# Kernel optimization log

Measured on AMD Instinct MI355X. Metric: run time of the kernel, lower is better.

## Reference

```python
import jax, jax.numpy as jnp
import numpy as np

T, B, XD, H, F = 1024, 256, 64, 256, 256  # seq_len, batch, x_dim, dim_RNN, feature dims
ALPHAS = [0.001, 0.01, 0.1]


def _alphas_per_unit():
    a = np.sort(np.asarray(ALPHAS, dtype=np.float32))
    assign = np.array([a[i % len(a)] for i in range(H)], dtype=np.float32)
    return jnp.asarray(np.sort(assign))  # [H]


def setup_inputs() -> dict:
    key = jax.random.key(0)
    ks = jax.random.split(key, 16)

    def w(k, shape, fan_in):
        return jax.random.normal(k, shape, jnp.float32) / np.sqrt(fan_in).astype(np.float32)

    return {
        "x": jax.random.normal(ks[0], (T, B, XD), jnp.float32),
        # feature_extractor_x: Linear(XD->F), Linear(F->F), tanh after each
        "Wx0": w(ks[1], (F, XD), XD), "bx0": jnp.zeros((F,), jnp.float32),
        "Wx1": w(ks[2], (F, F), F),   "bx1": jnp.zeros((F,), jnp.float32),
        # nn.RNN(F, H): tanh cell
        "Wih": w(ks[3], (H, F), F), "Whh": w(ks[4], (H, H), H),
        "bih": jnp.zeros((H,), jnp.float32), "bhh": jnp.zeros((H,), jnp.float32),
        # mlp_h_x: Linear(H->F), Linear(F->F), tanh after each
        "Wh0": w(ks[5], (F, H), H), "bh0": jnp.zeros((F,), jnp.float32),
        "Wh1": w(ks[6], (F, F), F), "bh1": jnp.zeros((F,), jnp.float32),
        # gen_out: Linear(F->XD)
        "Wg": w(ks[7], (XD, F), F), "bg": jnp.zeros((XD,), jnp.float32),
    }


def reference(x, Wx0, bx0, Wx1, bx1, Wih, Whh, bih, bhh, Wh0, bh0, Wh1, bh1, Wg, bg):
    act = jnp.tanh
    alphas = _alphas_per_unit()  # [H]

    # feature extractor applied to all timesteps at once (non-autonomous path)
    feat = act(jnp.einsum('tbx,fx->tbf', x, Wx0) + bx0)
    feat = act(jnp.einsum('tbf,gf->tbg', feat, Wx1) + bx1)  # [T,B,F]

    def step(h, ft):
        # y_t is generated from h BEFORE the recurrence update
        d = act(h @ Wh0.T + bh0)
        d = act(d @ Wh1.T + bh1)
        y = d @ Wg.T + bg  # [B,XD]
        h_raw = jnp.tanh(ft @ Wih.T + bih + h @ Whh.T + bhh)
        h_new = (1.0 - alphas) * h + alphas * h_raw  # leaky alpha-blend
        return h_new, y

    h0 = jnp.zeros((B, H), x.dtype)
    _, y = jax.lax.scan(step, h0, feat)  # y: [T,B,XD]
    return y
```

## Files before the change

### kernel.cpp

```cpp
#include <hip/hip_runtime.h>
#include <cstddef>


typedef _Float16 halfx8 __attribute__((ext_vector_type(8)));
typedef _Float16 halfx4 __attribute__((ext_vector_type(4)));
typedef float    f32x4  __attribute__((ext_vector_type(4)));

#define T_LEN 1024
#define B_SZ  256
#define H_DIM 256
#define M_ROWS (T_LEN * B_SZ)

__device__ __forceinline__ float fast_tanh(float x) {
  float e = __expf(2.0f * x);
  return 1.0f - 2.0f / (e + 1.0f);
}

__device__ __forceinline__ float alpha_of(int j) {
  return (j < 86) ? 0.001f : ((j < 171) ? 0.01f : 0.1f);
}

__device__ __forceinline__ void lds_barrier() {
  asm volatile("s_waitcnt lgkmcnt(0)\n\ts_barrier" ::: "memory");
}

template <int KCH, bool TANH>
__global__ __launch_bounds__(512, 2)
void gemm_f16(const float* A, const float* __restrict__ W,
              const float* __restrict__ bias, float* C, int mtiles) {
  constexpr int K  = KCH * 32;
  constexpr int KP = K + 8;
  __shared__ __attribute__((aligned(16))) _Float16 Ah[32][KP];

  const int tid  = threadIdx.x;
  const int lane = tid & 63;
  const int wave = tid >> 6;
  const int l15  = lane & 15;
  const int quad = lane >> 4;
  const int jw   = wave * 32;

  halfx8 Bf[2][KCH];
  float  bcol[2];
  int    jj[2];
#pragma unroll
  for (int nt = 0; nt < 2; nt++) {
    jj[nt]   = jw + nt * 16 + l15;
    bcol[nt] = bias[jj[nt]];
#pragma unroll
    for (int ks = 0; ks < KCH; ks++) {
      const float* wp = W + (size_t)jj[nt] * K + ks * 32 + quad * 8;
      float4 w0 = *(const float4*)wp;
      float4 w1 = *(const float4*)(wp + 4);
      halfx8 f;
      f[0] = (_Float16)w0.x; f[1] = (_Float16)w0.y;
      f[2] = (_Float16)w0.z; f[3] = (_Float16)w0.w;
      f[4] = (_Float16)w1.x; f[5] = (_Float16)w1.y;
      f[6] = (_Float16)w1.z; f[7] = (_Float16)w1.w;
      Bf[nt][ks] = f;
    }
  }

  const int srow = tid >> 4;
  const int sk4  = tid & 15;
  constexpr int SEG = K / 64;

  for (int bm = blockIdx.x; bm < mtiles; bm += gridDim.x) {
    const float* Ab = A + (size_t)bm * 32 * K;
    float4 tv[SEG];
#pragma unroll
    for (int s = 0; s < SEG; s++)
      tv[s] = *(const float4*)(Ab + (size_t)srow * K + (sk4 + s * 16) * 4);
#pragma unroll
    for (int s = 0; s < SEG; s++) {
      halfx4 h;
      h[0] = (_Float16)tv[s].x; h[1] = (_Float16)tv[s].y;
      h[2] = (_Float16)tv[s].z; h[3] = (_Float16)tv[s].w;
      *(halfx4*)&Ah[srow][(sk4 + s * 16) * 4] = h;
    }
    lds_barrier();

    f32x4 acc[2][2];
#pragma unroll
    for (int mi = 0; mi < 2; mi++)
#pragma unroll
      for (int nt = 0; nt < 2; nt++) acc[mi][nt] = (f32x4){0.f, 0.f, 0.f, 0.f};

#pragma unroll
    for (int ks = 0; ks < KCH; ks++)
#pragma unroll
      for (int mi = 0; mi < 2; mi++) {
        halfx8 a = *(const halfx8*)&Ah[mi * 16 + l15][ks * 32 + quad * 8];
#pragma unroll
        for (int nt = 0; nt < 2; nt++)
          acc[mi][nt] = __builtin_amdgcn_mfma_f32_16x16x32_f16(a, Bf[nt][ks], acc[mi][nt], 0, 0, 0);
      }

#pragma unroll
    for (int mi = 0; mi < 2; mi++)
#pragma unroll
      for (int nt = 0; nt < 2; nt++)
#pragma unroll
        for (int rg = 0; rg < 4; rg++) {
          const int rowg = bm * 32 + mi * 16 + quad * 4 + rg;
          float v = acc[mi][nt][rg] + bcol[nt];
          if (TANH) v = fast_tanh(v);
          C[(size_t)rowg * 256 + jj[nt]] = v;
        }
    lds_barrier();
  }
}

__global__ __launch_bounds__(256, 2)
void gemm_f16_out(const float* __restrict__ A, const float* __restrict__ W,
                  const float* __restrict__ bias, float* __restrict__ C,
                  int mtiles) {
  constexpr int K = 256, KCH = 8, KP = 264;
  __shared__ __attribute__((aligned(16))) _Float16 Ah[32][KP];

  const int tid  = threadIdx.x;
  const int lane = tid & 63;
  const int wave = tid >> 6;
  const int l15  = lane & 15;
  const int quad = lane >> 4;
  const int jcol = wave * 16 + l15;

  halfx8 Bf[KCH];
  const float bc = bias[jcol];
#pragma unroll
  for (int ks = 0; ks < KCH; ks++) {
    const float* wp = W + (size_t)jcol * K + ks * 32 + quad * 8;
    float4 w0 = *(const float4*)wp;
    float4 w1 = *(const float4*)(wp + 4);
    halfx8 f;
    f[0] = (_Float16)w0.x; f[1] = (_Float16)w0.y;
    f[2] = (_Float16)w0.z; f[3] = (_Float16)w0.w;
    f[4] = (_Float16)w1.x; f[5] = (_Float16)w1.y;
    f[6] = (_Float16)w1.z; f[7] = (_Float16)w1.w;
    Bf[ks] = f;
  }

  const int srow = tid >> 3;
  const int sk4  = tid & 7;

  for (int bm = blockIdx.x; bm < mtiles; bm += gridDim.x) {
    const float* Ab = A + (size_t)bm * 32 * K;
    float4 tv[8];
#pragma unroll
    for (int s = 0; s < 8; s++)
      tv[s] = *(const float4*)(Ab + (size_t)srow * K + (sk4 + s * 8) * 4);
#pragma unroll
    for (int s = 0; s < 8; s++) {
      halfx4 h;
      h[0] = (_Float16)tv[s].x; h[1] = (_Float16)tv[s].y;
      h[2] = (_Float16)tv[s].z; h[3] = (_Float16)tv[s].w;
      *(halfx4*)&Ah[srow][(sk4 + s * 8) * 4] = h;
    }
    lds_barrier();

    f32x4 acc[2];
#pragma unroll
    for (int mi = 0; mi < 2; mi++) acc[mi] = (f32x4){0.f, 0.f, 0.f, 0.f};
#pragma unroll
    for (int ks = 0; ks < KCH; ks++)
#pragma unroll
      for (int mi = 0; mi < 2; mi++) {
        halfx8 a = *(const halfx8*)&Ah[mi * 16 + l15][ks * 32 + quad * 8];
        acc[mi] = __builtin_amdgcn_mfma_f32_16x16x32_f16(a, Bf[ks], acc[mi], 0, 0, 0);
      }

#pragma unroll
    for (int mi = 0; mi < 2; mi++)
#pragma unroll
      for (int rg = 0; rg < 4; rg++) {
        const int rowg = bm * 32 + mi * 16 + quad * 4 + rg;
        C[(size_t)rowg * 64 + jcol] = acc[mi][rg] + bc;
      }
    lds_barrier();
  }
}

__global__ __launch_bounds__(1024, 4)
void rnn_serial(float* __restrict__ zx_hall,
                const float* __restrict__ Whh,
                const float* __restrict__ bhh_p)
{
  __shared__ __attribute__((aligned(16))) _Float16 hB[2][16][264];

  const int tid  = threadIdx.x;
  const int lane = tid & 63;
  const int wave = tid >> 6;
  const int l15  = lane & 15;
  const int quad = lane >> 4;
  const int r0   = blockIdx.x * 16;
  const int jcol = wave * 16 + l15;

  halfx8 Bf[8];
#pragma unroll
  for (int ks = 0; ks < 8; ks++) {
    const float* wp = Whh + (size_t)jcol * H_DIM + ks * 32 + quad * 8;
    float4 w0 = *(const float4*)wp;
    float4 w1 = *(const float4*)(wp + 4);
    halfx8 f;
    f[0] = (_Float16)w0.x; f[1] = (_Float16)w0.y;
    f[2] = (_Float16)w0.z; f[3] = (_Float16)w0.w;
    f[4] = (_Float16)w1.x; f[5] = (_Float16)w1.y;
    f[6] = (_Float16)w1.z; f[7] = (_Float16)w1.w;
    Bf[ks] = f;
  }
  const float bj  = bhh_p[jcol];
  const float aj  = alpha_of(jcol);
  const float oma = 1.0f - aj;

  for (int i = tid; i < 16 * 264; i += 1024) (&hB[0][0][0])[i] = (_Float16)0.0f;
  __syncthreads();

  float  hreg[4], zc[4];
  size_t zoff[4];
#pragma unroll
  for (int rg = 0; rg < 4; rg++) {
    hreg[rg] = 0.0f;
    zoff[rg] = (size_t)(r0 + quad * 4 + rg) * H_DIM + jcol;
    zc[rg]   = zx_hall[zoff[rg]];
  }

  int p = 0;
  for (int t = 0; t < T_LEN; t++) {
    f32x4 accE = {0.f, 0.f, 0.f, 0.f}, accO = {0.f, 0.f, 0.f, 0.f};
#pragma unroll
    for (int ks = 0; ks < 8; ks += 2) {
      halfx8 aE = *(const halfx8*)&hB[p][l15][ks * 32 + quad * 8];
      halfx8 aO = *(const halfx8*)&hB[p][l15][(ks + 1) * 32 + quad * 8];
      accE = __builtin_amdgcn_mfma_f32_16x16x32_f16(aE, Bf[ks],     accE, 0, 0, 0);
      accO = __builtin_amdgcn_mfma_f32_16x16x32_f16(aO, Bf[ks + 1], accO, 0, 0, 0);
    }

    const size_t tb = (size_t)((t + 1 < T_LEN) ? t + 1 : t) * (B_SZ * H_DIM);
    float zn[4];
#pragma unroll
    for (int rg = 0; rg < 4; rg++) zn[rg] = zx_hall[tb + zoff[rg]];

    const size_t tcur = (size_t)t * (B_SZ * H_DIM);
#pragma unroll
    for (int rg = 0; rg < 4; rg++) {
      const int r = quad * 4 + rg;
      float ho = hreg[rg];
      float hr = fast_tanh(zc[rg] + accE[rg] + accO[rg] + bj);
      float hn = oma * ho + aj * hr;
      zx_hall[tcur + zoff[rg]] = ho;
      hreg[rg] = hn;
      hB[p ^ 1][r][jcol] = (_Float16)hn;
    }

    lds_barrier();
    p ^= 1;
#pragma unroll
    for (int rg = 0; rg < 4; rg++) zc[rg] = zn[rg];
  }
}

extern "C" void kernel_launch(void* const* d_in, const int* in_sizes, int n_in,
                              void* d_out, int out_size, void* d_ws, size_t ws_size,
                              hipStream_t stream) {
  const float* x   = (const float*)d_in[0];
  const float* Wx0 = (const float*)d_in[1];
  const float* bx0 = (const float*)d_in[2];
  const float* Wx1 = (const float*)d_in[3];
  const float* bx1 = (const float*)d_in[4];
  const float* Wih = (const float*)d_in[5];
  const float* Whh = (const float*)d_in[6];
  const float* bih = (const float*)d_in[7];
  const float* bhh = (const float*)d_in[8];
  const float* Wh0 = (const float*)d_in[9];
  const float* bh0 = (const float*)d_in[10];
  const float* Wh1 = (const float*)d_in[11];
  const float* bh1 = (const float*)d_in[12];
  const float* Wg  = (const float*)d_in[13];
  const float* bg  = (const float*)d_in[14];
  float* out = (float*)d_out;

  float* buf = (float*)d_ws;
  const int MT = M_ROWS / 32;

  gemm_f16<2, true><<<512, 512, 0, stream>>>(x, Wx0, bx0, buf, MT);
  gemm_f16<8, true><<<512, 512, 0, stream>>>(buf, Wx1, bx1, buf, MT);
  gemm_f16<8, false><<<512, 512, 0, stream>>>(buf, Wih, bih, buf, MT);
  rnn_serial<<<16, 1024, 0, stream>>>(buf, Whh, bhh);
  gemm_f16<8, true><<<512, 512, 0, stream>>>(buf, Wh0, bh0, buf, MT);
  gemm_f16<8, true><<<512, 512, 0, stream>>>(buf, Wh1, bh1, buf, MT);
  gemm_f16_out<<<512, 256, 0, stream>>>(buf, Wg, bg, out, MT);
}
```

Baseline: 1.630 ms.

## Store intermediates in fp16 with transposed zx layout and streamlined RNN loop

```diff
diff --git a/kernel.cpp b/kernel.cpp
--- a/kernel.cpp
+++ b/kernel.cpp
@@ -24,10 +24,10 @@
   asm volatile("s_waitcnt lgkmcnt(0)\n\ts_barrier" ::: "memory");
 }
 
-template <int KCH, bool TANH>
+template <int KCH, bool TANH, bool INF32, bool ZXT>
 __global__ __launch_bounds__(512, 2)
-void gemm_f16(const float* A, const float* __restrict__ W,
-              const float* __restrict__ bias, float* C, int mtiles) {
+void gemm8(const void* __restrict__ Ap, const float* __restrict__ W,
+           const float* __restrict__ bias, void* __restrict__ Cp, int mtiles) {
   constexpr int K  = KCH * 32;
   constexpr int KP = K + 8;
   __shared__ __attribute__((aligned(16))) _Float16 Ah[32][KP];
@@ -62,20 +62,32 @@
 
   const int srow = tid >> 4;
   const int sk4  = tid & 15;
-  constexpr int SEG = K / 64;
 
   for (int bm = blockIdx.x; bm < mtiles; bm += gridDim.x) {
-    const float* Ab = A + (size_t)bm * 32 * K;
-    float4 tv[SEG];
-#pragma unroll
-    for (int s = 0; s < SEG; s++)
-      tv[s] = *(const float4*)(Ab + (size_t)srow * K + (sk4 + s * 16) * 4);
-#pragma unroll
-    for (int s = 0; s < SEG; s++) {
-      halfx4 h;
-      h[0] = (_Float16)tv[s].x; h[1] = (_Float16)tv[s].y;
-      h[2] = (_Float16)tv[s].z; h[3] = (_Float16)tv[s].w;
-      *(halfx4*)&Ah[srow][(sk4 + s * 16) * 4] = h;
+    if constexpr (INF32) {
+      const float* A = (const float*)Ap + (size_t)bm * 32 * K;
+      constexpr int SEG = K / 64;
+      float4 tv[SEG];
+#pragma unroll
+      for (int s = 0; s < SEG; s++)
+        tv[s] = *(const float4*)(A + (size_t)srow * K + (sk4 + s * 16) * 4);
+#pragma unroll
+      for (int s = 0; s < SEG; s++) {
+        halfx4 h;
+        h[0] = (_Float16)tv[s].x; h[1] = (_Float16)tv[s].y;
+        h[2] = (_Float16)tv[s].z; h[3] = (_Float16)tv[s].w;
+        *(halfx4*)&Ah[srow][(sk4 + s * 16) * 4] = h;
+      }
+    } else {
+      const _Float16* A = (const _Float16*)Ap + (size_t)bm * 32 * K;
+      constexpr int SEG = K / 128;
+      halfx8 tv[SEG];
+#pragma unroll
+      for (int s = 0; s < SEG; s++)
+        tv[s] = *(const halfx8*)(A + (size_t)srow * K + (sk4 + s * 16) * 8);
+#pragma unroll
+      for (int s = 0; s < SEG; s++)
+        *(halfx8*)&Ah[srow][(sk4 + s * 16) * 8] = tv[s];
     }
     lds_barrier();
 
@@ -95,25 +107,41 @@
           acc[mi][nt] = __builtin_amdgcn_mfma_f32_16x16x32_f16(a, Bf[nt][ks], acc[mi][nt], 0, 0, 0);
       }
 
-#pragma unroll
-    for (int mi = 0; mi < 2; mi++)
-#pragma unroll
-      for (int nt = 0; nt < 2; nt++)
-#pragma unroll
-        for (int rg = 0; rg < 4; rg++) {
-          const int rowg = bm * 32 + mi * 16 + quad * 4 + rg;
-          float v = acc[mi][nt][rg] + bcol[nt];
-          if (TANH) v = fast_tanh(v);
-          C[(size_t)rowg * 256 + jj[nt]] = v;
+    if constexpr (ZXT) {
+      _Float16* C = (_Float16*)Cp;
+      const size_t tb = (size_t)(bm >> 3) * (H_DIM * B_SZ) + (bm & 7) * 32 + quad * 4;
+#pragma unroll
+      for (int mi = 0; mi < 2; mi++)
+#pragma unroll
+        for (int nt = 0; nt < 2; nt++) {
+          halfx4 o;
+#pragma unroll
+          for (int rg = 0; rg < 4; rg++)
+            o[rg] = (_Float16)(acc[mi][nt][rg] + bcol[nt]);
+          *(halfx4*)(C + tb + (size_t)jj[nt] * B_SZ + mi * 16) = o;
         }
+    } else {
+      _Float16* C = (_Float16*)Cp;
+#pragma unroll
+      for (int mi = 0; mi < 2; mi++)
+#pragma unroll
+        for (int nt = 0; nt < 2; nt++)
+#pragma unroll
+          for (int rg = 0; rg < 4; rg++) {
+            const int rowg = bm * 32 + mi * 16 + quad * 4 + rg;
+            float v = acc[mi][nt][rg] + bcol[nt];
+            if (TANH) v = fast_tanh(v);
+            C[(size_t)rowg * 256 + jj[nt]] = (_Float16)v;
+          }
+    }
     lds_barrier();
   }
 }
 
 __global__ __launch_bounds__(256, 2)
-void gemm_f16_out(const float* __restrict__ A, const float* __restrict__ W,
-                  const float* __restrict__ bias, float* __restrict__ C,
-                  int mtiles) {
+void gemm4_out(const _Float16* __restrict__ A, const float* __restrict__ W,
+               const float* __restrict__ bias, float* __restrict__ C,
+               int mtiles) {
   constexpr int K = 256, KCH = 8, KP = 264;
   __shared__ __attribute__((aligned(16))) _Float16 Ah[32][KP];
 
@@ -140,21 +168,17 @@
   }
 
   const int srow = tid >> 3;
-  const int sk4  = tid & 7;
+  const int sk   = tid & 7;
 
   for (int bm = blockIdx.x; bm < mtiles; bm += gridDim.x) {
-    const float* Ab = A + (size_t)bm * 32 * K;
-    float4 tv[8];
-#pragma unroll
-    for (int s = 0; s < 8; s++)
-      tv[s] = *(const float4*)(Ab + (size_t)srow * K + (sk4 + s * 8) * 4);
-#pragma unroll
-    for (int s = 0; s < 8; s++) {
-      halfx4 h;
-      h[0] = (_Float16)tv[s].x; h[1] = (_Float16)tv[s].y;
-      h[2] = (_Float16)tv[s].z; h[3] = (_Float16)tv[s].w;
-      *(halfx4*)&Ah[srow][(sk4 + s * 8) * 4] = h;
-    }
+    const _Float16* Ab = A + (size_t)bm * 32 * K;
+    halfx8 tv[4];
+#pragma unroll
+    for (int s = 0; s < 4; s++)
+      tv[s] = *(const halfx8*)(Ab + (size_t)srow * K + (sk + s * 8) * 8);
+#pragma unroll
+    for (int s = 0; s < 4; s++)
+      *(halfx8*)&Ah[srow][(sk + s * 8) * 8] = tv[s];
     lds_barrier();
 
     f32x4 acc[2];
@@ -180,7 +204,8 @@
 }
 
 __global__ __launch_bounds__(1024, 4)
-void rnn_serial(float* __restrict__ zx_hall,
+void rnn_serial(const _Float16* __restrict__ zxT,
+                _Float16* __restrict__ h_all,
                 const float* __restrict__ Whh,
                 const float* __restrict__ bhh_p)
 {
@@ -214,47 +239,62 @@
   for (int i = tid; i < 16 * 264; i += 1024) (&hB[0][0][0])[i] = (_Float16)0.0f;
   __syncthreads();
 
-  float  hreg[4], zc[4];
-  size_t zoff[4];
-#pragma unroll
-  for (int rg = 0; rg < 4; rg++) {
-    hreg[rg] = 0.0f;
-    zoff[rg] = (size_t)(r0 + quad * 4 + rg) * H_DIM + jcol;
-    zc[rg]   = zx_hall[zoff[rg]];
-  }
-
-  int p = 0;
-  for (int t = 0; t < T_LEN; t++) {
-    f32x4 accE = {0.f, 0.f, 0.f, 0.f}, accO = {0.f, 0.f, 0.f, 0.f};
-#pragma unroll
-    for (int ks = 0; ks < 8; ks += 2) {
-      halfx8 aE = *(const halfx8*)&hB[p][l15][ks * 32 + quad * 8];
-      halfx8 aO = *(const halfx8*)&hB[p][l15][(ks + 1) * 32 + quad * 8];
-      accE = __builtin_amdgcn_mfma_f32_16x16x32_f16(aE, Bf[ks],     accE, 0, 0, 0);
-      accO = __builtin_amdgcn_mfma_f32_16x16x32_f16(aO, Bf[ks + 1], accO, 0, 0, 0);
-    }
-
-    const size_t tb = (size_t)((t + 1 < T_LEN) ? t + 1 : t) * (B_SZ * H_DIM);
-    float zn[4];
-#pragma unroll
-    for (int rg = 0; rg < 4; rg++) zn[rg] = zx_hall[tb + zoff[rg]];
-
-    const size_t tcur = (size_t)t * (B_SZ * H_DIM);
+  const _Float16* rdp[2] = {&hB[0][l15][quad * 8], &hB[1][l15][quad * 8]};
+  _Float16*       wrp[2] = {&hB[1][quad * 4][jcol], &hB[0][quad * 4][jcol]};
+
+  const _Float16* zp = zxT + (size_t)jcol * B_SZ + r0 + quad * 4;
+  _Float16*       hp = h_all + (size_t)(r0 + quad * 4) * H_DIM + jcol;
+  constexpr int STRIDE = B_SZ * H_DIM;
+
+  float  zc[4];
+  halfx4 zA;
+  {
+    halfx4 z0 = *(const halfx4*)zp;
+    zA = *(const halfx4*)(zp + STRIDE);
+    zp += 2 * (size_t)STRIDE;
+#pragma unroll
+    for (int rg = 0; rg < 4; rg++) zc[rg] = (float)z0[rg];
+  }
+
+  float    hreg[4] = {0.f, 0.f, 0.f, 0.f};
+  _Float16 hh[4]   = {(_Float16)0.f, (_Float16)0.f, (_Float16)0.f, (_Float16)0.f};
+
+  auto step = [&](int p) {
+    halfx4 znew = *(const halfx4*)zp;
+    zp += STRIDE;
+
+    f32x4 acc = {0.f, 0.f, 0.f, 0.f};
+    const _Float16* rd = rdp[p];
+#pragma unroll
+    for (int ks = 0; ks < 8; ks++) {
+      halfx8 a = *(const halfx8*)(rd + ks * 32);
+      acc = __builtin_amdgcn_mfma_f32_16x16x32_f16(a, Bf[ks], acc, 0, 0, 0);
+    }
+
+    _Float16* wr = wrp[p];
 #pragma unroll
     for (int rg = 0; rg < 4; rg++) {
-      const int r = quad * 4 + rg;
       float ho = hreg[rg];
-      float hr = fast_tanh(zc[rg] + accE[rg] + accO[rg] + bj);
+      float hr = fast_tanh(zc[rg] + acc[rg] + bj);
       float hn = oma * ho + aj * hr;
-      zx_hall[tcur + zoff[rg]] = ho;
+      hp[rg * H_DIM] = hh[rg];
       hreg[rg] = hn;
-      hB[p ^ 1][r][jcol] = (_Float16)hn;
-    }
-
-    lds_barrier();
-    p ^= 1;
-#pragma unroll
-    for (int rg = 0; rg < 4; rg++) zc[rg] = zn[rg];
+      _Float16 hf = (_Float16)hn;
+      hh[rg] = hf;
+      wr[rg * 264] = hf;
+    }
+    hp += STRIDE;
+
+    lds_barrier();
+
+#pragma unroll
+    for (int rg = 0; rg < 4; rg++) zc[rg] = (float)zA[rg];
+    zA = znew;
+  };
+
+  for (int it = 0; it < T_LEN / 2; ++it) {
+    step(0);
+    step(1);
   }
 }
 
@@ -278,14 +318,16 @@
   const float* bg  = (const float*)d_in[14];
   float* out = (float*)d_out;
 
-  float* buf = (float*)d_ws;
+  _Float16* bufA = (_Float16*)d_ws;
+  _Float16* bufB = bufA + (size_t)M_ROWS * 256;
+
   const int MT = M_ROWS / 32;
 
-  gemm_f16<2, true><<<512, 512, 0, stream>>>(x, Wx0, bx0, buf, MT);
-  gemm_f16<8, true><<<512, 512, 0, stream>>>(buf, Wx1, bx1, buf, MT);
-  gemm_f16<8, false><<<512, 512, 0, stream>>>(buf, Wih, bih, buf, MT);
-  rnn_serial<<<16, 1024, 0, stream>>>(buf, Whh, bhh);
-  gemm_f16<8, true><<<512, 512, 0, stream>>>(buf, Wh0, bh0, buf, MT);
-  gemm_f16<8, true><<<512, 512, 0, stream>>>(buf, Wh1, bh1, buf, MT);
-  gemm_f16_out<<<512, 256, 0, stream>>>(buf, Wg, bg, out, MT);
-}
+  gemm8<2, true, true, false><<<512, 512, 0, stream>>>(x, Wx0, bx0, bufA, MT);
+  gemm8<8, true, false, false><<<512, 512, 0, stream>>>(bufA, Wx1, bx1, bufB, MT);
+  gemm8<8, false, false, true><<<512, 512, 0, stream>>>(bufB, Wih, bih, bufA, MT);
+  rnn_serial<<<16, 1024, 0, stream>>>(bufA, bufB, Whh, bhh);
+  gemm8<8, true, false, false><<<512, 512, 0, stream>>>(bufB, Wh0, bh0, bufA, MT);
+  gemm8<8, true, false, false><<<512, 512, 0, stream>>>(bufA, Wh1, bh1, bufB, MT);
+  gemm4_out<<<512, 256, 0, stream>>>(bufB, Wg, bg, out, MT);
+}
```

Result: faster. 1.463 ms (-10.3%).
